# Optimization experiments

Measured on AMD Instinct MI355X. Metric: run time of the kernel, lower is better.

Reference implementation:

```python
import jax, jax.numpy as jnp
import numpy as np

N = 200000   # nodes
E = 6400000  # edges (avg degree 32)
T = 6        # member feature dim
M = 10       # fingerprint dim
L = 4        # R + 1 layers
GIN = 14     # group_level_input
GLO = 10     # group_level_output


def setup_inputs() -> dict:
    key = jax.random.key(0)
    ks = jax.random.split(key, 10)
    return {
        "x_member": jax.random.normal(ks[0], (N, T), dtype=jnp.float32),
        "x_group": jax.random.normal(ks[1], (1, GIN), dtype=jnp.float32),
        "src": jax.random.randint(ks[2], (E,), 0, N, dtype=jnp.int32),
        "dst": jax.random.randint(ks[3], (E,), 0, N, dtype=jnp.int32),
        "H": jax.random.normal(ks[4], (L, T, M), dtype=jnp.float32),
        "W": jax.random.normal(ks[5], (L,), dtype=jnp.float32),
        "gW": jax.random.normal(ks[6], (GLO, GIN), dtype=jnp.float32) * 0.1,
        "gb": jax.random.normal(ks[7], (GLO,), dtype=jnp.float32),
        "mW": jax.random.normal(ks[8], (3, M + GLO), dtype=jnp.float32) * 0.1,
        "mb": jax.random.normal(ks[9], (3,), dtype=jnp.float32),
    }


def reference(x_member, x_group, src, dst, H, W, gW, gb, mW, mb):
    n = x_member.shape[0]
    # message passing: neighbor feature sum per destination node  [N, T]
    neigh = jax.ops.segment_sum(x_member[src], dst, num_segments=n)
    v1 = x_member + neigh  # r[a] + sum of neighbor r's; r is layer-invariant
    # all R+1 layers at once: [L, N, M]
    v2 = jax.nn.sigmoid(jnp.einsum("nt,ltm->lnm", v1, H))
    fl = jax.nn.softmax(v2 * W[:, None, None], axis=-1)
    # f starts at zeros and accumulates softmax over every node and layer -> [1, M]
    f = jnp.sum(fl, axis=(0, 1))[None, :]
    # group-level perceptron
    g = jax.nn.sigmoid(x_group @ gW.T + gb)  # [1, GLO]
    merged = jnp.concatenate([f, g], axis=1)  # [1, M+GLO]
    return jax.nn.softmax(merged @ mW.T + mb, axis=-1)  # [1, 3]
```

## Files before the change

### kernel.cpp

```cpp
#include <hip/hip_runtime.h>
#include <hip/hip_fp16.h>
#include <math.h>

#define TDIM 6
#define MDIM 10
#define LDIM 4
#define GIND 14
#define GLOD 10

#define BINSHIFT 8
#define BINSZ 256
#define MAXBINS 1024

#define SC2_BLOCKS 512
#define SC2_THREADS 512
#define SC2_KQ 7
#define OVF_ENT 16384
#define META2 2048

#define SC_BLOCK 512
#define SC_EPT 32
#define SC_EPB (SC_BLOCK * SC_EPT)
#define AC_BLOCK 512
#define AC_CAP 8704
#define AC_EPT 17

__global__ void zero32_k(unsigned* __restrict__ p, int n) {
    int i = blockIdx.x * blockDim.x + threadIdx.x;
    if (i < n) p[i] = 0u;
}

__device__ __forceinline__ void add_row4(uint4 r, float& s0, float& s1, float& s2,
                                         float& s3, float& s4, float& s5) {
    float2 a0 = __half22float2(*(__half2*)&r.x);
    float2 a1 = __half22float2(*(__half2*)&r.y);
    float2 a2 = __half22float2(*(__half2*)&r.z);
    s0 += a0.x; s1 += a0.y; s2 += a1.x; s3 += a1.y; s4 += a2.x; s5 += a2.y;
}


__global__ __launch_bounds__(SC2_THREADS) void scat2_k(
        const float* __restrict__ xm, int N, uint4* __restrict__ xh,
        const int* __restrict__ src, const int* __restrict__ dst, int E, int NQ, int QPB,
        unsigned* __restrict__ gcount, unsigned* __restrict__ ebuf, int C, int nbins,
        uint2* __restrict__ ovf, unsigned* __restrict__ ocur) {
    __shared__ unsigned lcount[MAXBINS];
    __shared__ unsigned lbase[MAXBINS];
    int tid = threadIdx.x;
    for (int i = tid; i < MAXBINS; i += SC2_THREADS) lcount[i] = 0u;

    int gid = blockIdx.x * SC2_THREADS + tid;
    int gstride = gridDim.x * SC2_THREADS;
    for (int n = gid; n < N; n += gstride) {
        const float2* r = (const float2*)(xm + (size_t)n * TDIM);
        float2 a = r[0], b = r[1], c = r[2];
        __half2 h0 = __floats2half2_rn(a.x, a.y);
        __half2 h1 = __floats2half2_rn(b.x, b.y);
        __half2 h2 = __floats2half2_rn(c.x, c.y);
        uint4 o;
        o.x = *(unsigned*)&h0; o.y = *(unsigned*)&h1; o.z = *(unsigned*)&h2; o.w = 0u;
        xh[n] = o;
    }
    if (blockIdx.x == 0) {
        for (int e = NQ * 4 + tid; e < E; e += SC2_THREADS) {
            unsigned oc = atomicAdd(ocur, 1u);
            if (oc < OVF_ENT) ovf[oc] = make_uint2((unsigned)src[e], (unsigned)dst[e]);
        }
    }
    __syncthreads();

    int qb = blockIdx.x * QPB;
    int qend = qb + QPB; if (qend > NQ) qend = NQ;
    const int4* s4p = (const int4*)src;
    const int4* d4p = (const int4*)dst;

    unsigned pk[SC2_KQ * 4];
    unsigned wr[SC2_KQ * 4];

#pragma unroll
    for (int i = 0; i < SC2_KQ; i++) {
        int q = qb + tid + i * SC2_THREADS;
        if (q < qend) {
            int4 sv = s4p[q];
            int4 dv = d4p[q];
            {
                unsigned du = (unsigned)dv.x, b = du >> BINSHIFT;
                pk[i*4+0] = ((du & (BINSZ-1)) << 18) | (unsigned)sv.x;
                wr[i*4+0] = (b << 18) | atomicAdd(&lcount[b], 1u);
            }
            {
                unsigned du = (unsigned)dv.y, b = du >> BINSHIFT;
                pk[i*4+1] = ((du & (BINSZ-1)) << 18) | (unsigned)sv.y;
                wr[i*4+1] = (b << 18) | atomicAdd(&lcount[b], 1u);
            }
            {
                unsigned du = (unsigned)dv.z, b = du >> BINSHIFT;
                pk[i*4+2] = ((du & (BINSZ-1)) << 18) | (unsigned)sv.z;
                wr[i*4+2] = (b << 18) | atomicAdd(&lcount[b], 1u);
            }
            {
                unsigned du = (unsigned)dv.w, b = du >> BINSHIFT;
                pk[i*4+3] = ((du & (BINSZ-1)) << 18) | (unsigned)sv.w;
                wr[i*4+3] = (b << 18) | atomicAdd(&lcount[b], 1u);
            }
        } else {
            pk[i*4+0] = 0xFFFFFFFFu; pk[i*4+1] = 0xFFFFFFFFu;
            pk[i*4+2] = 0xFFFFFFFFu; pk[i*4+3] = 0xFFFFFFFFu;
        }
    }
    __syncthreads();

    for (int i = tid; i < nbins; i += SC2_THREADS) {
        unsigned c = lcount[i];
        if (c) lbase[i] = atomicAdd(&gcount[i], c);
    }
    __syncthreads();

#pragma unroll
    for (int k = 0; k < SC2_KQ * 4; k++) {
        unsigned p = pk[k];
        if (p != 0xFFFFFFFFu) {
            unsigned b = wr[k] >> 18;
            unsigned pos = lbase[b] + (wr[k] & 0x3FFFFu);
            if (pos < (unsigned)C) {
                ebuf[b * (unsigned)C + pos] = p;
            } else {
                unsigned oc = atomicAdd(ocur, 1u);
                if (oc < OVF_ENT) {
                    unsigned s = p & 0x3FFFFu;
                    unsigned d = (b << BINSHIFT) | (p >> 18);
                    ovf[oc] = make_uint2(s, d);
                }
            }
        }
    }
}

__global__ __launch_bounds__(AC_BLOCK) void accum2_k(
        const float* __restrict__ xm, const uint4* __restrict__ xh,
        const unsigned* __restrict__ ebuf, const unsigned* __restrict__ gcount, int C,
        const unsigned* __restrict__ ocur, const uint2* __restrict__ ovf,
        const float* __restrict__ H, const float* __restrict__ W,
        float* __restrict__ facc, int N) {
    __shared__ unsigned srt[AC_CAP];
    __shared__ unsigned cnt[BINSZ];
    __shared__ unsigned cstart[BINSZ];
    __shared__ unsigned wsum[8];
    __shared__ unsigned ovl[256];
    __shared__ unsigned ovn;
    __shared__ float sH[LDIM * TDIM * MDIM];
    __shared__ float sW[LDIM];
    __shared__ float sred[AC_BLOCK / 64][MDIM];
    float (*part)[BINSZ][TDIM] = (float(*)[BINSZ][TDIM])srt;
    int tid = threadIdx.x;
    int bin = blockIdx.x;
    for (int i = tid; i < LDIM * TDIM * MDIM; i += AC_BLOCK) sH[i] = H[i];
    if (tid < LDIM) sW[tid] = W[tid];
    if (tid < BINSZ) cnt[tid] = 0u;
    if (tid == 0) ovn = 0u;
    __syncthreads();

    unsigned gc = gcount[bin];
    unsigned m = gc < (unsigned)C ? gc : (unsigned)C;
    unsigned e0 = (unsigned)bin * (unsigned)C;
    int nbase = bin << BINSHIFT;

    unsigned ed_[AC_EPT];
    unsigned rk_[AC_EPT];
#pragma unroll
    for (int k = 0; k < AC_EPT; k++) {
        unsigned i = (unsigned)tid + (unsigned)k * AC_BLOCK;
        if (i < m) {
            unsigned v = __builtin_nontemporal_load(ebuf + e0 + i);
            ed_[k] = v;
            rk_[k] = atomicAdd(&cnt[v >> 18], 1u);
        }
    }
    {
        unsigned novf = *ocur;
        if (novf > OVF_ENT) novf = OVF_ENT;
        for (unsigned i = tid; i < novf; i += AC_BLOCK) {
            uint2 e = ovf[i];
            if ((e.y >> BINSHIFT) == (unsigned)bin) {
                unsigned u = atomicAdd(&ovn, 1u);
                if (u < 256u) ovl[u] = ((e.y & (BINSZ-1)) << 18) | e.x;
            }
        }
    }
    __syncthreads();

    {
        unsigned v = (tid < BINSZ) ? cnt[tid] : 0u;
        int lane = tid & 63;
#pragma unroll
        for (int off = 1; off < 64; off <<= 1) {
            unsigned t = (unsigned)__shfl_up((int)v, off, 64);
            if (lane >= off) v += t;
        }
        if (tid < BINSZ && lane == 63) wsum[tid >> 6] = v;
        __syncthreads();
        if (tid < BINSZ) {
            unsigned add = 0;
            int w = tid >> 6;
#pragma unroll
            for (int ww = 0; ww < 3; ww++) if (ww < w) add += wsum[ww];
            cstart[tid] = v + add - cnt[tid];
        }
        __syncthreads();
    }

#pragma unroll
    for (int k = 0; k < AC_EPT; k++) {
        unsigned i = (unsigned)tid + (unsigned)k * AC_BLOCK;
        if (i < m) {
            unsigned v = ed_[k];
            srt[cstart[v >> 18] + rk_[k]] = v & 0x3FFFFu;
        }
    }
    __syncthreads();

    int node = tid & (BINSZ - 1);
    int role = tid >> 8;
    int n = nbase + node;
    float s0 = 0.f, s1 = 0.f, s2 = 0.f, s3 = 0.f, s4 = 0.f, s5 = 0.f;
    if (n < N) {
        unsigned c = cnt[node];
        unsigned b0 = cstart[node];
        unsigned h = c >> 1;
        unsigned j  = role ? h : 0u;
        unsigned je = role ? c : h;
        for (; j + 8 <= je; j += 8) {
            unsigned i0 = srt[b0 + j],     i1 = srt[b0 + j + 1];
            unsigned i2 = srt[b0 + j + 2], i3 = srt[b0 + j + 3];
            unsigned i4 = srt[b0 + j + 4], i5 = srt[b0 + j + 5];
            unsigned i6 = srt[b0 + j + 6], i7 = srt[b0 + j + 7];
            uint4 r0 = xh[i0], r1 = xh[i1], r2 = xh[i2], r3 = xh[i3];
            uint4 r4 = xh[i4], r5 = xh[i5], r6 = xh[i6], r7 = xh[i7];
            add_row4(r0, s0, s1, s2, s3, s4, s5);
            add_row4(r1, s0, s1, s2, s3, s4, s5);
            add_row4(r2, s0, s1, s2, s3, s4, s5);
            add_row4(r3, s0, s1, s2, s3, s4, s5);
            add_row4(r4, s0, s1, s2, s3, s4, s5);
            add_row4(r5, s0, s1, s2, s3, s4, s5);
            add_row4(r6, s0, s1, s2, s3, s4, s5);
            add_row4(r7, s0, s1, s2, s3, s4, s5);
        }
        for (; j + 2 <= je; j += 2) {
            unsigned ia = srt[b0 + j], ib = srt[b0 + j + 1];
            uint4 ra = xh[ia], rb = xh[ib];
            add_row4(ra, s0, s1, s2, s3, s4, s5);
            add_row4(rb, s0, s1, s2, s3, s4, s5);
        }
        if (j < je) {
            uint4 ra = xh[srt[b0 + j]];
            add_row4(ra, s0, s1, s2, s3, s4, s5);
        }
        if (role == 0) {
            unsigned no = ovn < 256u ? ovn : 256u;
            for (unsigned q = 0; q < no; q++) {
                unsigned o = ovl[q];
                if ((int)(o >> 18) == node) {
                    uint4 rr = xh[o & 0x3FFFFu];
                    add_row4(rr, s0, s1, s2, s3, s4, s5);
                }
            }
        }
    }
    __syncthreads();
    part[role][node][0] = s0; part[role][node][1] = s1; part[role][node][2] = s2;
    part[role][node][3] = s3; part[role][node][4] = s4; part[role][node][5] = s5;
    __syncthreads();

    float fs[MDIM];
#pragma unroll
    for (int mm = 0; mm < MDIM; mm++) fs[mm] = 0.f;

    if (n < N) {
        float v[TDIM];
        const float2* xr = (const float2*)(xm + (size_t)n * TDIM);
        float2 x0 = xr[0], x1 = xr[1], x2 = xr[2];
        v[0] = x0.x + part[0][node][0] + part[1][node][0];
        v[1] = x0.y + part[0][node][1] + part[1][node][1];
        v[2] = x1.x + part[0][node][2] + part[1][node][2];
        v[3] = x1.y + part[0][node][3] + part[1][node][3];
        v[4] = x2.x + part[0][node][4] + part[1][node][4];
        v[5] = x2.y + part[0][node][5] + part[1][node][5];

        int lb = role << 1;
#pragma unroll
        for (int li = 0; li < 2; li++) {
            int l = lb + li;
            float z[MDIM];
#pragma unroll
            for (int mm = 0; mm < MDIM; mm++) {
                float a2 = 0.f;
#pragma unroll
                for (int t = 0; t < TDIM; t++) a2 += v[t] * sH[(l * TDIM + t) * MDIM + mm];
                z[mm] = a2;
            }
            float wl = sW[l];
            float mx = -1e30f;
#pragma unroll
            for (int mm = 0; mm < MDIM; mm++) {
                float sg = wl / (1.f + __expf(-z[mm]));
                z[mm] = sg;
                mx = fmaxf(mx, sg);
            }
            float se = 0.f;
#pragma unroll
            for (int mm = 0; mm < MDIM; mm++) {
                float e = __expf(z[mm] - mx);
                z[mm] = e;
                se += e;
            }
            float inv = 1.f / se;
#pragma unroll
            for (int mm = 0; mm < MDIM; mm++) fs[mm] += z[mm] * inv;
        }
    }

#pragma unroll
    for (int mm = 0; mm < MDIM; mm++) {
        float v = fs[mm];
#pragma unroll
        for (int off = 32; off > 0; off >>= 1) v += __shfl_down(v, off, 64);
        fs[mm] = v;
    }
    int wave = tid >> 6, lane = tid & 63;
    if (lane == 0) {
#pragma unroll
        for (int mm = 0; mm < MDIM; mm++) sred[wave][mm] = fs[mm];
    }
    __syncthreads();
    if (tid < MDIM) {
        float s = 0.f;
#pragma unroll
        for (int w = 0; w < AC_BLOCK / 64; w++) s += sred[w][tid];
        atomicAdd(facc + tid, s);
    }
}


__global__ __launch_bounds__(256) void prep_k(const float* __restrict__ xm, int N,
                                              uint4* __restrict__ xh,
                                              const int* __restrict__ dst, int E,
                                              unsigned* __restrict__ hist, int nbins) {
    __shared__ unsigned lh[MAXBINS];
    for (int i = threadIdx.x; i < MAXBINS; i += blockDim.x) lh[i] = 0u;
    __syncthreads();
    int gid = blockIdx.x * blockDim.x + threadIdx.x;
    int gstride = gridDim.x * blockDim.x;
    for (int n = gid; n < N; n += gstride) {
        const float2* r = (const float2*)(xm + (size_t)n * TDIM);
        float2 a = r[0], b = r[1], c = r[2];
        __half2 h0 = __floats2half2_rn(a.x, a.y);
        __half2 h1 = __floats2half2_rn(b.x, b.y);
        __half2 h2 = __floats2half2_rn(c.x, c.y);
        uint4 o;
        o.x = *(unsigned*)&h0; o.y = *(unsigned*)&h1; o.z = *(unsigned*)&h2; o.w = 0u;
        xh[n] = o;
    }
    int e4 = E >> 2;
    const int4* d4p = (const int4*)dst;
    for (int i = gid; i < e4; i += gstride) {
        int4 d = d4p[i];
        atomicAdd(&lh[((unsigned)d.x) >> BINSHIFT], 1u);
        atomicAdd(&lh[((unsigned)d.y) >> BINSHIFT], 1u);
        atomicAdd(&lh[((unsigned)d.z) >> BINSHIFT], 1u);
        atomicAdd(&lh[((unsigned)d.w) >> BINSHIFT], 1u);
    }
    for (int e = (e4 << 2) + gid; e < E; e += gstride)
        atomicAdd(&lh[((unsigned)dst[e]) >> BINSHIFT], 1u);
    __syncthreads();
    for (int i = threadIdx.x; i < nbins; i += blockDim.x)
        if (lh[i]) atomicAdd(&hist[i], lh[i]);
}

__global__ __launch_bounds__(MAXBINS) void scan_k(const unsigned* __restrict__ hist,
                                                  unsigned* __restrict__ offsets,
                                                  unsigned* __restrict__ gfill, int nbins) {
    __shared__ unsigned buf[2][MAXBINS];
    int t = threadIdx.x;
    buf[0][t] = (t < nbins) ? hist[t] : 0u;
    __syncthreads();
    int cur = 0;
    for (int off = 1; off < MAXBINS; off <<= 1) {
        unsigned v = buf[cur][t];
        if (t >= off) v += buf[cur][t - off];
        buf[cur ^ 1][t] = v;
        __syncthreads();
        cur ^= 1;
    }
    if (t < nbins) {
        unsigned ex = t ? buf[cur][t - 1] : 0u;
        offsets[t] = ex;
        gfill[t] = ex;
    }
    if (t == 0) offsets[nbins] = buf[cur][nbins - 1];
}

__global__ __launch_bounds__(SC_BLOCK) void scatter_k(const int* __restrict__ src,
                                                      const int* __restrict__ dst, int E,
                                                      unsigned* __restrict__ gfill,
                                                      unsigned* __restrict__ ebuf, int nbins) {
    __shared__ unsigned lcount[MAXBINS];
    __shared__ unsigned lbase[MAXBINS];
    for (int i = threadIdx.x; i < MAXBINS; i += SC_BLOCK) lcount[i] = 0u;
    __syncthreads();
    int base = blockIdx.x * SC_EPB + threadIdx.x * SC_EPT;
    int s[SC_EPT], d[SC_EPT];
    unsigned rk[SC_EPT];
#pragma unroll
    for (int q = 0; q < SC_EPT / 4; q++) {
        int e = base + q * 4;
        if (e + 3 < E) {
            int4 s4 = *(const int4*)(src + e);
            int4 d4 = *(const int4*)(dst + e);
            s[q*4+0] = s4.x; s[q*4+1] = s4.y; s[q*4+2] = s4.z; s[q*4+3] = s4.w;
            d[q*4+0] = d4.x; d[q*4+1] = d4.y; d[q*4+2] = d4.z; d[q*4+3] = d4.w;
        } else {
#pragma unroll
            for (int k = 0; k < 4; k++) {
                int ee = e + k;
                s[q*4+k] = (ee < E) ? src[ee] : -1;
                d[q*4+k] = (ee < E) ? dst[ee] : 0;
            }
        }
    }
#pragma unroll
    for (int k = 0; k < SC_EPT; k++)
        if (s[k] >= 0) rk[k] = atomicAdd(&lcount[((unsigned)d[k]) >> BINSHIFT], 1u);
    __syncthreads();
    for (int i = threadIdx.x; i < nbins; i += SC_BLOCK) {
        unsigned c = lcount[i];
        if (c) lbase[i] = atomicAdd(&gfill[i], c);
    }
    __syncthreads();
#pragma unroll
    for (int k = 0; k < SC_EPT; k++) {
        if (s[k] >= 0) {
            unsigned du = (unsigned)d[k];
            unsigned b = du >> BINSHIFT;
            unsigned pack = ((du & (BINSZ - 1)) << 18) | (unsigned)s[k];
            ebuf[lbase[b] + rk[k]] = pack;
        }
    }
}

__global__ __launch_bounds__(AC_BLOCK) void accum_node_k(
        const float* __restrict__ xm, const uint4* __restrict__ xh,
        const unsigned* __restrict__ ebuf, const unsigned* __restrict__ offsets,
        const float* __restrict__ H, const float* __restrict__ W,
        float* __restrict__ facc, int N) {
    __shared__ unsigned srt[AC_CAP];
    __shared__ unsigned cnt[BINSZ];
    __shared__ unsigned tmp[BINSZ];
    __shared__ unsigned cstart[BINSZ];
    __shared__ float sH[LDIM * TDIM * MDIM];
    __shared__ float sW[LDIM];
    __shared__ float sred[AC_BLOCK / 64][MDIM];
    int tid = threadIdx.x;
    int bin = blockIdx.x;
    for (int i = tid; i < LDIM * TDIM * MDIM; i += AC_BLOCK) sH[i] = H[i];
    if (tid < LDIM) sW[tid] = W[tid];
    if (tid < BINSZ) cnt[tid] = 0u;
    __syncthreads();

    unsigned e0 = offsets[bin], e1 = offsets[bin + 1];
    unsigned total = e1 - e0;
    unsigned m = total < AC_CAP ? total : AC_CAP;
    int nbase = bin << BINSHIFT;

    unsigned ed_[AC_EPT];
    unsigned rk_[AC_EPT];
#pragma unroll
    for (int k = 0; k < AC_EPT; k++) {
        unsigned idx = e0 + (unsigned)tid + (unsigned)k * AC_BLOCK;
        if (idx < e0 + m) {
            unsigned v = ebuf[idx];
            ed_[k] = v;
            rk_[k] = atomicAdd(&cnt[v >> 18], 1u);
        }
    }
    __syncthreads();

    if (tid < BINSZ) tmp[tid] = cnt[tid];
    __syncthreads();
    for (int off = 1; off < BINSZ; off <<= 1) {
        unsigned v = 0;
        if (tid < BINSZ) { v = tmp[tid]; if (tid >= off) v += tmp[tid - off]; }
        __syncthreads();
        if (tid < BINSZ) tmp[tid] = v;
        __syncthreads();
    }
    if (tid < BINSZ) cstart[tid] = tmp[tid] - cnt[tid];
    __syncthreads();

#pragma unroll
    for (int k = 0; k < AC_EPT; k++) {
        unsigned idx = e0 + (unsigned)tid + (unsigned)k * AC_BLOCK;
        if (idx < e0 + m) {
            unsigned v = ed_[k];
            srt[cstart[v >> 18] + rk_[k]] = v & 0x3FFFFu;
        }
    }
    __syncthreads();

    float fs[MDIM];
#pragma unroll
    for (int mm = 0; mm < MDIM; mm++) fs[mm] = 0.f;

    int n = nbase + tid;
    if (tid < BINSZ && n < N) {
        float s0 = 0.f, s1 = 0.f, s2 = 0.f, s3 = 0.f, s4 = 0.f, s5 = 0.f;
        unsigned c = cnt[tid];
        unsigned b0 = cstart[tid];
        unsigned j = 0;
        for (; j + 2 <= c; j += 2) {
            unsigned sa = srt[b0 + j], sb = srt[b0 + j + 1];
            uint4 ra = xh[sa];
            uint4 rb = xh[sb];
            add_row4(ra, s0, s1, s2, s3, s4, s5);
            add_row4(rb, s0, s1, s2, s3, s4, s5);
        }
        if (j < c) {
            uint4 ra = xh[srt[b0 + j]];
            add_row4(ra, s0, s1, s2, s3, s4, s5);
        }
        for (unsigned idx = e0 + m; idx < e1; idx++) {
            unsigned v = ebuf[idx];
            if ((int)(v >> 18) == tid) {
                uint4 ra = xh[v & 0x3FFFFu];
                add_row4(ra, s0, s1, s2, s3, s4, s5);
            }
        }

        float v[TDIM];
        const float2* xr = (const float2*)(xm + (size_t)n * TDIM);
        float2 x0 = xr[0], x1 = xr[1], x2 = xr[2];
        v[0] = x0.x + s0; v[1] = x0.y + s1;
        v[2] = x1.x + s2; v[3] = x1.y + s3;
        v[4] = x2.x + s4; v[5] = x2.y + s5;

#pragma unroll
        for (int l = 0; l < LDIM; l++) {
            float z[MDIM];
#pragma unroll
            for (int mm = 0; mm < MDIM; mm++) {
                float a2 = 0.f;
#pragma unroll
                for (int t = 0; t < TDIM; t++) a2 += v[t] * sH[(l * TDIM + t) * MDIM + mm];
                z[mm] = a2;
            }
            float wl = sW[l];
            float mx = -1e30f;
#pragma unroll
            for (int mm = 0; mm < MDIM; mm++) {
                float sg = wl / (1.f + __expf(-z[mm]));
                z[mm] = sg;
                mx = fmaxf(mx, sg);
            }
            float se = 0.f;
#pragma unroll
            for (int mm = 0; mm < MDIM; mm++) {
                float e = __expf(z[mm] - mx);
                z[mm] = e;
                se += e;
            }
            float inv = 1.f / se;
#pragma unroll
            for (int mm = 0; mm < MDIM; mm++) fs[mm] += z[mm] * inv;
        }
    }

#pragma unroll
    for (int mm = 0; mm < MDIM; mm++) {
        float v = fs[mm];
#pragma unroll
        for (int off = 32; off > 0; off >>= 1) v += __shfl_down(v, off, 64);
        fs[mm] = v;
    }
    int wave = tid >> 6, lane = tid & 63;
    if (lane == 0) {
#pragma unroll
        for (int mm = 0; mm < MDIM; mm++) sred[wave][mm] = fs[mm];
    }
    __syncthreads();
    if (tid < MDIM) {
        float s = 0.f;
#pragma unroll
        for (int w = 0; w < AC_BLOCK / 64; w++) s += sred[w][tid];
        atomicAdd(facc + tid, s);
    }
}

__global__ void finalize_k(const float* __restrict__ facc,
                           const float* __restrict__ xg,
                           const float* __restrict__ gW,
                           const float* __restrict__ gb,
                           const float* __restrict__ mW,
                           const float* __restrict__ mb,
                           float* __restrict__ out) {
    if (threadIdx.x == 0 && blockIdx.x == 0) {
        float merged[MDIM + GLOD];
#pragma unroll
        for (int m = 0; m < MDIM; m++) merged[m] = facc[m];
        for (int j = 0; j < GLOD; j++) {
            float a = gb[j];
            for (int i = 0; i < GIND; i++) a += xg[i] * gW[j * GIND + i];
            merged[MDIM + j] = 1.f / (1.f + __expf(-a));
        }
        float lg[3];
        float mx = -1e30f;
        for (int k = 0; k < 3; k++) {
            float a = mb[k];
            for (int j = 0; j < MDIM + GLOD; j++) a += merged[j] * mW[k * (MDIM + GLOD) + j];
            lg[k] = a;
            mx = fmaxf(mx, a);
        }
        float se = 0.f;
        for (int k = 0; k < 3; k++) { lg[k] = __expf(lg[k] - mx); se += lg[k]; }
        float inv = 1.f / se;
        for (int k = 0; k < 3; k++) out[k] = lg[k] * inv;
    }
}

__global__ void fb_zero_k(float* __restrict__ ws, int n) {
    int i = blockIdx.x * blockDim.x + threadIdx.x;
    if (i < n) ws[i] = 0.f;
}

__global__ void fb_edge_scatter_k(const float* __restrict__ xm,
                                  const int* __restrict__ src,
                                  const int* __restrict__ dst,
                                  float* __restrict__ neigh, int E) {
    int e = blockIdx.x * blockDim.x + threadIdx.x;
    if (e >= E) return;
    int s = src[e], d = dst[e];
    const float2* r = (const float2*)(xm + (size_t)s * TDIM);
    float2 a = r[0], b = r[1], c = r[2];
    float* o = neigh + (size_t)d * TDIM;
    atomicAdd(o + 0, a.x); atomicAdd(o + 1, a.y);
    atomicAdd(o + 2, b.x); atomicAdd(o + 3, b.y);
    atomicAdd(o + 4, c.x); atomicAdd(o + 5, c.y);
}

__global__ __launch_bounds__(256) void fb_node_k(
        const float* __restrict__ xm, const float* __restrict__ neigh,
        const float* __restrict__ H, const float* __restrict__ W,
        float* __restrict__ facc, int N) {
    __shared__ float sH[LDIM * TDIM * MDIM];
    __shared__ float sW[LDIM];
    __shared__ float sred[4][MDIM];
    int tid = threadIdx.x;
    for (int i = tid; i < LDIM * TDIM * MDIM; i += blockDim.x) sH[i] = H[i];
    if (tid < LDIM) sW[tid] = W[tid];
    __syncthreads();
    float fs[MDIM];
#pragma unroll
    for (int m = 0; m < MDIM; m++) fs[m] = 0.f;
    for (int n = blockIdx.x * blockDim.x + tid; n < N; n += gridDim.x * blockDim.x) {
        float v[TDIM];
        const float2* xr = (const float2*)(xm + (size_t)n * TDIM);
        const float2* nr = (const float2*)(neigh + (size_t)n * TDIM);
#pragma unroll
        for (int t2 = 0; t2 < 3; t2++) {
            float2 a = xr[t2], b = nr[t2];
            v[2 * t2 + 0] = a.x + b.x;
            v[2 * t2 + 1] = a.y + b.y;
        }
#pragma unroll
        for (int l = 0; l < LDIM; l++) {
            float z[MDIM];
#pragma unroll
            for (int m = 0; m < MDIM; m++) {
                float a2 = 0.f;
#pragma unroll
                for (int t = 0; t < TDIM; t++) a2 += v[t] * sH[(l * TDIM + t) * MDIM + m];
                z[m] = a2;
            }
            float wl = sW[l], mx = -1e30f;
#pragma unroll
            for (int m = 0; m < MDIM; m++) { float sg = wl / (1.f + __expf(-z[m])); z[m] = sg; mx = fmaxf(mx, sg); }
            float se = 0.f;
#pragma unroll
            for (int m = 0; m < MDIM; m++) { float e = __expf(z[m] - mx); z[m] = e; se += e; }
            float inv = 1.f / se;
#pragma unroll
            for (int m = 0; m < MDIM; m++) fs[m] += z[m] * inv;
        }
    }
#pragma unroll
    for (int m = 0; m < MDIM; m++) {
        float v = fs[m];
#pragma unroll
        for (int off = 32; off > 0; off >>= 1) v += __shfl_down(v, off, 64);
        fs[m] = v;
    }
    int wave = tid >> 6, lane = tid & 63;
    if (lane == 0) {
#pragma unroll
        for (int m = 0; m < MDIM; m++) sred[wave][m] = fs[m];
    }
    __syncthreads();
    if (tid < MDIM) {
        float s = sred[0][tid] + sred[1][tid] + sred[2][tid] + sred[3][tid];
        atomicAdd(facc + tid, s);
    }
}

extern "C" void kernel_launch(void* const* d_in, const int* in_sizes, int n_in,
                              void* d_out, int out_size, void* d_ws, size_t ws_size,
                              hipStream_t stream) {
    const float* xm  = (const float*)d_in[0];
    const float* xg  = (const float*)d_in[1];
    const int*   src = (const int*)d_in[2];
    const int*   dst = (const int*)d_in[3];
    const float* H   = (const float*)d_in[4];
    const float* W   = (const float*)d_in[5];
    const float* gW  = (const float*)d_in[6];
    const float* gb  = (const float*)d_in[7];
    const float* mW  = (const float*)d_in[8];
    const float* mb  = (const float*)d_in[9];
    float* out = (float*)d_out;

    int N = in_sizes[0] / TDIM;
    int E = in_sizes[2];
    int nbins = (N + BINSZ - 1) >> BINSHIFT;
    size_t ws_words = ws_size / 4;
    size_t xh_words = (size_t)N * 4;

    long fixed = (long)(xh_words + META2 + (size_t)OVF_ENT * 2);
    long avail = (long)ws_words - fixed;
    long C = avail > 0 ? (avail / nbins) & ~3L : 0;
    if (C > AC_CAP) C = AC_CAP;
    double mu = (double)E / nbins;
    long Cmin = (long)(mu + 4.0 * sqrt(mu) + 32.0);
    int NQ = E >> 2;
    int QPB = (NQ + SC2_BLOCKS - 1) / SC2_BLOCKS;
    bool ok1 = (C >= Cmin) && nbins <= MAXBINS && N <= (1 << 18) &&
               QPB <= SC2_KQ * SC2_THREADS;

    size_t meta_words2 = MAXBINS + (MAXBINS + 1) + MAXBINS + 16;
    size_t need2 = (xh_words + (size_t)E + meta_words2) * 4;
    bool ok2 = ws_size >= need2 && nbins <= MAXBINS && N <= (1 << 18);

    if (ok1) {
        uint4*    xh     = (uint4*)d_ws;
        unsigned* ebuf   = (unsigned*)d_ws + xh_words;
        unsigned* gcount = ebuf + (size_t)nbins * C;
        unsigned* ocur   = gcount + MAXBINS;
        float*    facc   = (float*)(ocur + 16);
        uint2*    ovf    = (uint2*)(gcount + META2);

        zero32_k<<<(META2 + 255) / 256, 256, 0, stream>>>(gcount, META2);
        scat2_k<<<SC2_BLOCKS, SC2_THREADS, 0, stream>>>(xm, N, xh, src, dst, E, NQ, QPB,
                                                        gcount, ebuf, (int)C, nbins, ovf, ocur);
        accum2_k<<<nbins, AC_BLOCK, 0, stream>>>(xm, xh, ebuf, gcount, (int)C, ocur, ovf,
                                                 H, W, facc, N);
        finalize_k<<<1, 64, 0, stream>>>(facc, xg, gW, gb, mW, mb, out);
    } else if (ok2) {
        uint4*    xh      = (uint4*)d_ws;
        unsigned* ebuf    = (unsigned*)d_ws + xh_words;
        unsigned* hist    = ebuf + (size_t)E;
        unsigned* offsets = hist + MAXBINS;
        unsigned* gfill   = offsets + MAXBINS + 1;
        float*    facc    = (float*)(gfill + MAXBINS);

        zero32_k<<<(int)((meta_words2 + 255) / 256), 256, 0, stream>>>(hist, (int)meta_words2);
        prep_k<<<1024, 256, 0, stream>>>(xm, N, xh, dst, E, hist, nbins);
        scan_k<<<1, MAXBINS, 0, stream>>>(hist, offsets, gfill, nbins);
        scatter_k<<<(E + SC_EPB - 1) / SC_EPB, SC_BLOCK, 0, stream>>>(src, dst, E, gfill, ebuf, nbins);
        accum_node_k<<<nbins, AC_BLOCK, 0, stream>>>(xm, xh, ebuf, offsets, H, W, facc, N);
        finalize_k<<<1, 64, 0, stream>>>(facc, xg, gW, gb, mW, mb, out);
    } else {
        float* neigh = (float*)d_ws;
        float* facc  = neigh + (size_t)N * TDIM;
        int zn = N * TDIM + 16;
        fb_zero_k<<<(zn + 255) / 256, 256, 0, stream>>>(neigh, zn);
        fb_edge_scatter_k<<<(E + 255) / 256, 256, 0, stream>>>(xm, src, dst, neigh, E);
        fb_node_k<<<256, 256, 0, stream>>>(xm, neigh, H, W, facc, N);
        finalize_k<<<1, 64, 0, stream>>>(facc, xg, gW, gb, mW, mb, out);
    }
}
```

Before: 134.3 us.

## Stage scatter writes through shared-memory bin sort for coalesced global stores

The scatter kernel now first counts the destination bins for its whole range. It then processes edges in chunks, counting-sorts each chunk by bin in shared memory with a block-wide prefix scan, and writes to the global edge buffer in sorted order. The aim is to turn random scattered 4-byte stores into mostly contiguous runs per bin, which should improve write coalescing. In exchange, dst is read twice, there are more barriers, and about 45KB of extra LDS is used, which may lower occupancy.

```diff
diff --git a/kernel.cpp b/kernel.cpp
--- a/kernel.cpp
+++ b/kernel.cpp
@@ -14,7 +14,9 @@
 
 #define SC2_BLOCKS 512
 #define SC2_THREADS 512
-#define SC2_KQ 7
+#define SC2_CHQ 1408
+#define SC2_CHUNKS 3
+#define SC2_TQ 3
 #define OVF_ENT 16384
 #define META2 2048
 
@@ -46,8 +48,13 @@
         uint2* __restrict__ ovf, unsigned* __restrict__ ocur) {
     __shared__ unsigned lcount[MAXBINS];
     __shared__ unsigned lbase[MAXBINS];
+    __shared__ unsigned lcur[MAXBINS];
+    __shared__ unsigned cstart[MAXBINS];
+    __shared__ unsigned wsum[8];
+    __shared__ unsigned spk[SC2_CHQ * 4];
+    __shared__ unsigned sgp[SC2_CHQ * 4];
     int tid = threadIdx.x;
-    for (int i = tid; i < MAXBINS; i += SC2_THREADS) lcount[i] = 0u;
+    for (int i = tid; i < MAXBINS; i += SC2_THREADS) { lcount[i] = 0u; lcur[i] = 0u; }
 
     int gid = blockIdx.x * SC2_THREADS + tid;
     int gstride = gridDim.x * SC2_THREADS;
@@ -74,65 +81,113 @@
     const int4* s4p = (const int4*)src;
     const int4* d4p = (const int4*)dst;
 
-    unsigned pk[SC2_KQ * 4];
-    unsigned wr[SC2_KQ * 4];
-
-#pragma unroll
-    for (int i = 0; i < SC2_KQ; i++) {
-        int q = qb + tid + i * SC2_THREADS;
-        if (q < qend) {
-            int4 sv = s4p[q];
-            int4 dv = d4p[q];
-            {
-                unsigned du = (unsigned)dv.x, b = du >> BINSHIFT;
-                pk[i*4+0] = ((du & (BINSZ-1)) << 18) | (unsigned)sv.x;
-                wr[i*4+0] = (b << 18) | atomicAdd(&lcount[b], 1u);
-            }
-            {
-                unsigned du = (unsigned)dv.y, b = du >> BINSHIFT;
-                pk[i*4+1] = ((du & (BINSZ-1)) << 18) | (unsigned)sv.y;
-                wr[i*4+1] = (b << 18) | atomicAdd(&lcount[b], 1u);
-            }
-            {
-                unsigned du = (unsigned)dv.z, b = du >> BINSHIFT;
-                pk[i*4+2] = ((du & (BINSZ-1)) << 18) | (unsigned)sv.z;
-                wr[i*4+2] = (b << 18) | atomicAdd(&lcount[b], 1u);
-            }
-            {
-                unsigned du = (unsigned)dv.w, b = du >> BINSHIFT;
-                pk[i*4+3] = ((du & (BINSZ-1)) << 18) | (unsigned)sv.w;
-                wr[i*4+3] = (b << 18) | atomicAdd(&lcount[b], 1u);
-            }
-        } else {
-            pk[i*4+0] = 0xFFFFFFFFu; pk[i*4+1] = 0xFFFFFFFFu;
-            pk[i*4+2] = 0xFFFFFFFFu; pk[i*4+3] = 0xFFFFFFFFu;
-        }
-    }
-    __syncthreads();
-
+    for (int q = qb + tid; q < qend; q += SC2_THREADS) {
+        int4 dv = d4p[q];
+        atomicAdd(&lcount[((unsigned)dv.x) >> BINSHIFT], 1u);
+        atomicAdd(&lcount[((unsigned)dv.y) >> BINSHIFT], 1u);
+        atomicAdd(&lcount[((unsigned)dv.z) >> BINSHIFT], 1u);
+        atomicAdd(&lcount[((unsigned)dv.w) >> BINSHIFT], 1u);
+    }
+    __syncthreads();
     for (int i = tid; i < nbins; i += SC2_THREADS) {
         unsigned c = lcount[i];
         if (c) lbase[i] = atomicAdd(&gcount[i], c);
     }
     __syncthreads();
 
-#pragma unroll
-    for (int k = 0; k < SC2_KQ * 4; k++) {
-        unsigned p = pk[k];
-        if (p != 0xFFFFFFFFu) {
-            unsigned b = wr[k] >> 18;
-            unsigned pos = lbase[b] + (wr[k] & 0x3FFFFu);
-            if (pos < (unsigned)C) {
-                ebuf[b * (unsigned)C + pos] = p;
+    for (int ch = 0; ch < SC2_CHUNKS; ch++) {
+        int cb = qb + ch * SC2_CHQ;
+        if (cb >= qend) break;
+        int ce = cb + SC2_CHQ; if (ce > qend) ce = qend;
+        for (int i = tid; i < MAXBINS; i += SC2_THREADS) lcount[i] = 0u;
+        __syncthreads();
+
+        unsigned pk[SC2_TQ * 4];
+        unsigned wr[SC2_TQ * 4];
+#pragma unroll
+        for (int i = 0; i < SC2_TQ; i++) {
+            int q = cb + tid + i * SC2_THREADS;
+            if (q < ce) {
+                int4 sv = s4p[q];
+                int4 dv = d4p[q];
+                {
+                    unsigned du = (unsigned)dv.x, b = du >> BINSHIFT;
+                    pk[i*4+0] = ((du & (BINSZ-1)) << 18) | (unsigned)sv.x;
+                    wr[i*4+0] = (b << 18) | atomicAdd(&lcount[b], 1u);
+                }
+                {
+                    unsigned du = (unsigned)dv.y, b = du >> BINSHIFT;
+                    pk[i*4+1] = ((du & (BINSZ-1)) << 18) | (unsigned)sv.y;
+                    wr[i*4+1] = (b << 18) | atomicAdd(&lcount[b], 1u);
+                }
+                {
+                    unsigned du = (unsigned)dv.z, b = du >> BINSHIFT;
+                    pk[i*4+2] = ((du & (BINSZ-1)) << 18) | (unsigned)sv.z;
+                    wr[i*4+2] = (b << 18) | atomicAdd(&lcount[b], 1u);
+                }
+                {
+                    unsigned du = (unsigned)dv.w, b = du >> BINSHIFT;
+                    pk[i*4+3] = ((du & (BINSZ-1)) << 18) | (unsigned)sv.w;
+                    wr[i*4+3] = (b << 18) | atomicAdd(&lcount[b], 1u);
+                }
             } else {
-                unsigned oc = atomicAdd(ocur, 1u);
-                if (oc < OVF_ENT) {
-                    unsigned s = p & 0x3FFFFu;
-                    unsigned d = (b << BINSHIFT) | (p >> 18);
-                    ovf[oc] = make_uint2(s, d);
+                pk[i*4+0] = 0xFFFFFFFFu; pk[i*4+1] = 0xFFFFFFFFu;
+                pk[i*4+2] = 0xFFFFFFFFu; pk[i*4+3] = 0xFFFFFFFFu;
+            }
+        }
+        __syncthreads();
+
+        unsigned a0 = lcount[2*tid], a1 = lcount[2*tid+1];
+        {
+            unsigned s = a0 + a1;
+            int lane = tid & 63;
+#pragma unroll
+            for (int off = 1; off < 64; off <<= 1) {
+                unsigned t = (unsigned)__shfl_up((int)s, off, 64);
+                if (lane >= off) s += t;
+            }
+            if (lane == 63) wsum[tid >> 6] = s;
+            __syncthreads();
+            unsigned add = 0; int w = tid >> 6;
+#pragma unroll
+            for (int ww = 0; ww < 7; ww++) if (ww < w) add += wsum[ww];
+            unsigned excl = s + add - (a0 + a1);
+            cstart[2*tid] = excl;
+            cstart[2*tid+1] = excl + a0;
+        }
+        __syncthreads();
+
+#pragma unroll
+        for (int k = 0; k < SC2_TQ * 4; k++) {
+            unsigned p = pk[k];
+            if (p != 0xFFFFFFFFu) {
+                unsigned b = wr[k] >> 18;
+                unsigned r = wr[k] & 0x3FFFFu;
+                unsigned li = cstart[b] + r;
+                unsigned pos = lbase[b] + lcur[b] + r;
+                if (pos < (unsigned)C) {
+                    spk[li] = p;
+                    sgp[li] = b * (unsigned)C + pos;
+                } else {
+                    spk[li] = 0xFFFFFFFFu;
+                    unsigned oc = atomicAdd(ocur, 1u);
+                    if (oc < OVF_ENT) {
+                        ovf[oc] = make_uint2(p & 0x3FFFFu,
+                                             (b << BINSHIFT) | (p >> 18));
+                    }
                 }
             }
         }
+        __syncthreads();
+
+        unsigned T = cstart[MAXBINS-1] + lcount[MAXBINS-1];
+        for (unsigned j = tid; j < T; j += SC2_THREADS) {
+            unsigned p = spk[j];
+            if (p != 0xFFFFFFFFu) ebuf[sgp[j]] = p;
+        }
+        lcur[2*tid]   += a0;
+        lcur[2*tid+1] += a1;
+        __syncthreads();
     }
 }
 
@@ -739,7 +794,7 @@
     int NQ = E >> 2;
     int QPB = (NQ + SC2_BLOCKS - 1) / SC2_BLOCKS;
     bool ok1 = (C >= Cmin) && nbins <= MAXBINS && N <= (1 << 18) &&
-               QPB <= SC2_KQ * SC2_THREADS;
+               QPB <= SC2_CHUNKS * SC2_CHQ;
 
     size_t meta_words2 = MAXBINS + (MAXBINS + 1) + MAXBINS + 16;
     size_t need2 = (xh_words + (size_t)E + meta_words2) * 4;
```

Result: faster. 114.3 us (-14.9%).
